# Kernel tuning notes

Measured on AMD Instinct MI355X. Metric: run time of the kernel, lower is better.

The kernel has to match this reference:

```python
import jax, jax.numpy as jnp
import numpy as np

TEMPERATURE = 0.5
EPS = 1e-8
NEG = -1e30  # effectively -inf for masked logits


def _l2norm(x):
    n = jnp.sqrt(jnp.sum(x * x, axis=1, keepdims=True))
    return x / jnp.maximum(n, EPS)


def setup_inputs() -> dict:
    key = jax.random.key(0)
    ks = jax.random.split(key, 4)
    N, D = 2048, 128
    return {f"projection_image_aug{i+1}": jax.random.normal(ks[i], (N, D), dtype=jnp.float32)
            for i in range(4)}


def reference(projection_image_aug1, projection_image_aug2,
              projection_image_aug3, projection_image_aug4):
    zs = [projection_image_aug1.astype(jnp.float32),
          projection_image_aug2.astype(jnp.float32),
          projection_image_aug3.astype(jnp.float32),
          projection_image_aug4.astype(jnp.float32)]
    N = zs[0].shape[0]
    k = len(zs)
    z = jnp.concatenate(zs[:2], axis=0)        # [2N, D]
    z_all = jnp.concatenate(zs, axis=0)        # [kN, D]
    # cosine sim via normalize + matmul (same math as broadcast CosineSimilarity)
    sim = _l2norm(z) @ _l2norm(z_all).T / TEMPERATURE   # [2N, kN]

    rows = jnp.arange(2 * N)
    half = rows // N                 # 0 for first N rows, 1 for second
    idx = rows % N
    cols = jnp.arange(k * N)
    block = cols // N
    # mask: diagonal entries of every N-block except the target block (1-half)
    diag = (cols[None, :] % N) == idx[:, None]
    mask = diag & (block[None, :] != (1 - half)[:, None])
    sim_m = jnp.where(mask, NEG, sim)
    # positive column: aug2 partner for rows<N, aug1 partner for rows>=N
    target_col = (1 - half) * N + idx
    pos = jnp.take_along_axis(sim_m, target_col[:, None], axis=1)[:, 0]
    # cross_entropy(reduction='sum') / (2N)
    loss = jnp.sum(jax.nn.logsumexp(sim_m, axis=1) - pos) / (2 * N)
    return loss
```

## Files before the change

### kernel.cpp

```cpp
#include <hip/hip_runtime.h>
#include <hip/hip_bf16.h>


#define NN      2048
#define DD      128
#define TWO_N   4096
#define FOUR_N  8192
#define BM      128
#define BN      128
#define CT      64

using frag_ab = __attribute__((ext_vector_type(8))) short;
using f32x4   = __attribute__((ext_vector_type(4))) float;

__device__ inline void gl_lds16(const short* g, short* l) {
  __builtin_amdgcn_global_load_lds(
      (const __attribute__((address_space(1))) void*)g,
      (__attribute__((address_space(3))) void*)l, 16, 0, 0);
}

__device__ inline int swz(int chunk) {
  return (chunk & ~15) | ((chunk & 15) ^ ((chunk >> 4) & 15));
}

__global__ __launch_bounds__(256) void knorm(const float* __restrict__ p0,
                                             const float* __restrict__ p1,
                                             const float* __restrict__ p2,
                                             const float* __restrict__ p3,
                                             short* __restrict__ Bn,
                                             float* __restrict__ out) {
  if (blockIdx.x == 0 && threadIdx.x == 0) out[0] = 0.0f;
  int wave = threadIdx.x >> 6, lane = threadIdx.x & 63;
  int row = blockIdx.x * 4 + wave;
  int q = row >> 11, idx = row & (NN - 1);
  const float* src = (q == 0) ? p0 : (q == 1) ? p1 : (q == 2) ? p2 : p3;
  const float2* s2 = (const float2*)(src + (size_t)idx * DD);
  float2 v = s2[lane];
  float ss = v.x * v.x + v.y * v.y;
  #pragma unroll
  for (int sh = 1; sh < 64; sh <<= 1) ss += __shfl_xor(ss, sh, 64);
  float inv = 1.0f / fmaxf(sqrtf(ss), 1e-8f);
  __hip_bfloat162 o;
  o.x = __float2bfloat16(v.x * inv);
  o.y = __float2bfloat16(v.y * inv);
  ((__hip_bfloat162*)(Bn + (size_t)row * DD))[lane] = o;
}

__global__ __launch_bounds__(256) void kgemm(const short* __restrict__ Bn,
                                             float* __restrict__ pS) {
  __shared__ short sA[BM * DD];
  __shared__ short sB[BN * DD];
  __shared__ float sS[BM][2];

  int t = threadIdx.x, wave = t >> 6, lane = t & 63;
  int quad = lane >> 4, l16 = lane & 15;

  const short* gA = Bn + (size_t)blockIdx.x * BM * DD;
  const short* gB = Bn + (size_t)blockIdx.y * BN * DD;
  #pragma unroll
  for (int i = 0; i < 8; ++i) {
    int c0 = i * 256 + wave * 64;
    gl_lds16(gA + (size_t)swz(c0 + lane) * 8, sA + (size_t)c0 * 8);
    gl_lds16(gB + (size_t)swz(c0 + lane) * 8, sB + (size_t)c0 * 8);
  }
  __syncthreads();

  int rowHalf = wave >> 1, colHalf = wave & 1;
  f32x4 acc[4][4];
  #pragma unroll
  for (int rf = 0; rf < 4; ++rf)
    #pragma unroll
    for (int cf = 0; cf < 4; ++cf) acc[rf][cf] = (f32x4){0.f, 0.f, 0.f, 0.f};

  #pragma unroll
  for (int k = 0; k < 4; ++k) {
    frag_ab a[4], b[4];
    #pragma unroll
    for (int rf = 0; rf < 4; ++rf) {
      int r_ = rowHalf * 64 + rf * 16 + l16;
      a[rf] = *(const frag_ab*)&sA[(size_t)((r_ << 4) | ((k * 4 + quad) ^ l16)) * 8];
    }
    #pragma unroll
    for (int cf = 0; cf < 4; ++cf) {
      int r_ = colHalf * 64 + cf * 16 + l16;
      b[cf] = *(const frag_ab*)&sB[(size_t)((r_ << 4) | ((k * 4 + quad) ^ l16)) * 8];
    }
    #pragma unroll
    for (int rf = 0; rf < 4; ++rf)
      #pragma unroll
      for (int cf = 0; cf < 4; ++cf)
        acc[rf][cf] = __builtin_amdgcn_mfma_f32_16x16x32_bf16(a[rf], b[cf], acc[rf][cf], 0, 0, 0);
  }

  int grBase = blockIdx.x * BM;
  #pragma unroll
  for (int rf = 0; rf < 4; ++rf) {
    #pragma unroll
    for (int r = 0; r < 4; ++r) {
      int rowLocal = rowHalf * 64 + rf * 16 + quad * 4 + r;
      float s = 0.f;
      #pragma unroll
      for (int cf = 0; cf < 4; ++cf)
        s += __expf(fmaf(acc[rf][cf][r], 2.0f, -2.0f));
      #pragma unroll
      for (int sh = 1; sh < 16; sh <<= 1) s += __shfl_xor(s, sh, 64);
      if (l16 == 0) sS[rowLocal][colHalf] = s;
    }
  }
  __syncthreads();
  if (t < BM)
    pS[(size_t)(grBase + t) * CT + blockIdx.y] = sS[t][0] + sS[t][1];
}

__global__ __launch_bounds__(256) void kfin(const short* __restrict__ Bn,
                                            const float* __restrict__ pS,
                                            float* __restrict__ out) {
  int t = threadIdx.x, wave = t >> 6, lane = t & 63;
  int grBase = blockIdx.x * BM;
  __shared__ float sRed[4];

  float wloss = 0.f;
  for (int rr = wave; rr < BM; rr += 4) {
    int gr = grBase + rr;
    int idx = gr & (NN - 1), half = gr >> 11;
    float S = pS[(size_t)gr * CT + lane];
    #pragma unroll
    for (int sh = 1; sh < 64; sh <<= 1) S += __shfl_xor(S, sh, 64);
    unsigned int ua = ((const unsigned int*)(Bn + (size_t)gr * DD))[lane];
    unsigned int ub = ((const unsigned int*)(Bn + (size_t)((1 - half) * NN + idx) * DD))[lane];
    unsigned int uc = ((const unsigned int*)(Bn + (size_t)(2 * NN + idx) * DD))[lane];
    unsigned int ud = ((const unsigned int*)(Bn + (size_t)(3 * NN + idx) * DD))[lane];
    float a0 = __uint_as_float((ua & 0xffffu) << 16), a1 = __uint_as_float(ua & 0xffff0000u);
    float b0 = __uint_as_float((ub & 0xffffu) << 16), b1 = __uint_as_float(ub & 0xffff0000u);
    float c0 = __uint_as_float((uc & 0xffffu) << 16), c1 = __uint_as_float(uc & 0xffff0000u);
    float d0 = __uint_as_float((ud & 0xffffu) << 16), d1 = __uint_as_float(ud & 0xffff0000u);
    float daa = a0 * a0 + a1 * a1;
    float dab = a0 * b0 + a1 * b1;
    float dac = a0 * c0 + a1 * c1;
    float dad = a0 * d0 + a1 * d1;
    #pragma unroll
    for (int sh = 1; sh < 64; sh <<= 1) {
      daa += __shfl_xor(daa, sh, 64);
      dab += __shfl_xor(dab, sh, 64);
      dac += __shfl_xor(dac, sh, 64);
      dad += __shfl_xor(dad, sh, 64);
    }
    float Sc = S - __expf(fmaf(daa, 2.0f, -2.0f))
                 - __expf(fmaf(dac, 2.0f, -2.0f))
                 - __expf(fmaf(dad, 2.0f, -2.0f));
    float loss = (2.0f + __logf(Sc)) - 2.0f * dab;
    if (lane == 0) wloss += loss;
  }
  if (lane == 0) sRed[wave] = wloss;
  __syncthreads();
  if (t == 0)
    atomicAdd(out, (sRed[0] + sRed[1] + sRed[2] + sRed[3]) * (1.0f / (float)TWO_N));
}

extern "C" void kernel_launch(void* const* d_in, const int* in_sizes, int n_in,
                              void* d_out, int out_size, void* d_ws, size_t ws_size,
                              hipStream_t stream) {
  (void)in_sizes; (void)n_in; (void)out_size; (void)ws_size;
  const float* p0 = (const float*)d_in[0];
  const float* p1 = (const float*)d_in[1];
  const float* p2 = (const float*)d_in[2];
  const float* p3 = (const float*)d_in[3];

  short* Bn = (short*)d_ws;
  float* pS = (float*)((char*)d_ws + (size_t)FOUR_N * DD * sizeof(short));
  float* out = (float*)d_out;

  knorm<<<FOUR_N / 4, 256, 0, stream>>>(p0, p1, p2, p3, Bn, out);
  kgemm<<<dim3(TWO_N / BM, FOUR_N / BN), 256, 0, stream>>>(Bn, pS);
  kfin<<<TWO_N / BM, 256, 0, stream>>>(Bn, pS, out);
}
```

Baseline: 110.4 us.

## Make GEMM blocks persistent over column tiles with double-buffered B loads

Each GEMM block now sweeps 8 consecutive 128-column tiles instead of one. The A fragments stay in registers across the sweep, and the next B tile is prefetched into a second LDS buffer while the current tile is multiplied. Per-row exp sums accumulate in registers, so the partial-sum buffer shrinks from 64 to 8 entries per row and the final kernel reduces fewer values. The aim is to cut block launch overhead, repeated A loads and the partial-sum traffic. The cost is a grid of only 256 blocks at one block per CU with 4 waves, which may leave MFMA and exp latency poorly hidden.

New measurement: 122.8 us. 11.2% more time.

```diff
diff --git a/kernel.cpp b/kernel.cpp
--- a/kernel.cpp
+++ b/kernel.cpp
@@ -8,7 +8,8 @@
 #define FOUR_N  8192
 #define BM      128
 #define BN      128
-#define CT      64
+#define GT      8
+#define CTG     8
 
 using frag_ab = __attribute__((ext_vector_type(8))) short;
 using f32x4   = __attribute__((ext_vector_type(4))) float;
@@ -46,70 +47,101 @@
   ((__hip_bfloat162*)(Bn + (size_t)row * DD))[lane] = o;
 }
 
-__global__ __launch_bounds__(256) void kgemm(const short* __restrict__ Bn,
-                                             float* __restrict__ pS) {
+__global__ __launch_bounds__(256, 1) void kgemm(const short* __restrict__ Bn,
+                                                float* __restrict__ pS) {
   __shared__ short sA[BM * DD];
-  __shared__ short sB[BN * DD];
+  __shared__ short sB[2][BN * DD];
   __shared__ float sS[BM][2];
 
   int t = threadIdx.x, wave = t >> 6, lane = t & 63;
   int quad = lane >> 4, l16 = lane & 15;
+  int rowHalf = wave >> 1, colHalf = wave & 1;
 
   const short* gA = Bn + (size_t)blockIdx.x * BM * DD;
-  const short* gB = Bn + (size_t)blockIdx.y * BN * DD;
+  const short* gB0 = Bn + (size_t)blockIdx.y * (GT * BN) * DD;
+
   #pragma unroll
   for (int i = 0; i < 8; ++i) {
     int c0 = i * 256 + wave * 64;
     gl_lds16(gA + (size_t)swz(c0 + lane) * 8, sA + (size_t)c0 * 8);
-    gl_lds16(gB + (size_t)swz(c0 + lane) * 8, sB + (size_t)c0 * 8);
+    gl_lds16(gB0 + (size_t)swz(c0 + lane) * 8, sB[0] + (size_t)c0 * 8);
   }
   __syncthreads();
 
-  int rowHalf = wave >> 1, colHalf = wave & 1;
-  f32x4 acc[4][4];
-  #pragma unroll
-  for (int rf = 0; rf < 4; ++rf)
-    #pragma unroll
-    for (int cf = 0; cf < 4; ++cf) acc[rf][cf] = (f32x4){0.f, 0.f, 0.f, 0.f};
-
-  #pragma unroll
-  for (int k = 0; k < 4; ++k) {
-    frag_ab a[4], b[4];
+  frag_ab a[4][4];
+  #pragma unroll
+  for (int k = 0; k < 4; ++k)
     #pragma unroll
     for (int rf = 0; rf < 4; ++rf) {
       int r_ = rowHalf * 64 + rf * 16 + l16;
-      a[rf] = *(const frag_ab*)&sA[(size_t)((r_ << 4) | ((k * 4 + quad) ^ l16)) * 8];
-    }
-    #pragma unroll
-    for (int cf = 0; cf < 4; ++cf) {
-      int r_ = colHalf * 64 + cf * 16 + l16;
-      b[cf] = *(const frag_ab*)&sB[(size_t)((r_ << 4) | ((k * 4 + quad) ^ l16)) * 8];
-    }
+      a[k][rf] = *(const frag_ab*)&sA[(size_t)((r_ << 4) | ((k * 4 + quad) ^ l16)) * 8];
+    }
+
+  float sAcc[4][4];
+  #pragma unroll
+  for (int rf = 0; rf < 4; ++rf)
+    #pragma unroll
+    for (int r = 0; r < 4; ++r) sAcc[rf][r] = 0.f;
+
+  #pragma unroll
+  for (int g = 0; g < GT; ++g) {
+    if (g < GT - 1) {
+      const short* gBn = gB0 + (size_t)(g + 1) * BN * DD;
+      short* dst = sB[(g + 1) & 1];
+      #pragma unroll
+      for (int i = 0; i < 8; ++i) {
+        int c0 = i * 256 + wave * 64;
+        gl_lds16(gBn + (size_t)swz(c0 + lane) * 8, dst + (size_t)c0 * 8);
+      }
+    }
+    const short* sBg = sB[g & 1];
+
+    f32x4 acc[4][4];
     #pragma unroll
     for (int rf = 0; rf < 4; ++rf)
       #pragma unroll
-      for (int cf = 0; cf < 4; ++cf)
-        acc[rf][cf] = __builtin_amdgcn_mfma_f32_16x16x32_bf16(a[rf], b[cf], acc[rf][cf], 0, 0, 0);
+      for (int cf = 0; cf < 4; ++cf) acc[rf][cf] = (f32x4){0.f, 0.f, 0.f, 0.f};
+
+    #pragma unroll
+    for (int k = 0; k < 4; ++k) {
+      frag_ab b[4];
+      #pragma unroll
+      for (int cf = 0; cf < 4; ++cf) {
+        int r_ = colHalf * 64 + cf * 16 + l16;
+        b[cf] = *(const frag_ab*)&sBg[(size_t)((r_ << 4) | ((k * 4 + quad) ^ l16)) * 8];
+      }
+      #pragma unroll
+      for (int rf = 0; rf < 4; ++rf)
+        #pragma unroll
+        for (int cf = 0; cf < 4; ++cf)
+          acc[rf][cf] = __builtin_amdgcn_mfma_f32_16x16x32_bf16(a[k][rf], b[cf], acc[rf][cf], 0, 0, 0);
+    }
+
+    #pragma unroll
+    for (int rf = 0; rf < 4; ++rf)
+      #pragma unroll
+      for (int r = 0; r < 4; ++r) {
+        float s = 0.f;
+        #pragma unroll
+        for (int cf = 0; cf < 4; ++cf)
+          s += __expf(fmaf(acc[rf][cf][r], 2.0f, -2.0f));
+        sAcc[rf][r] += s;
+      }
+    __syncthreads();
   }
 
-  int grBase = blockIdx.x * BM;
-  #pragma unroll
-  for (int rf = 0; rf < 4; ++rf) {
+  #pragma unroll
+  for (int rf = 0; rf < 4; ++rf)
     #pragma unroll
     for (int r = 0; r < 4; ++r) {
-      int rowLocal = rowHalf * 64 + rf * 16 + quad * 4 + r;
-      float s = 0.f;
-      #pragma unroll
-      for (int cf = 0; cf < 4; ++cf)
-        s += __expf(fmaf(acc[rf][cf][r], 2.0f, -2.0f));
+      float s = sAcc[rf][r];
       #pragma unroll
       for (int sh = 1; sh < 16; sh <<= 1) s += __shfl_xor(s, sh, 64);
-      if (l16 == 0) sS[rowLocal][colHalf] = s;
-    }
-  }
+      if (l16 == 0) sS[rowHalf * 64 + rf * 16 + quad * 4 + r][colHalf] = s;
+    }
   __syncthreads();
   if (t < BM)
-    pS[(size_t)(grBase + t) * CT + blockIdx.y] = sS[t][0] + sS[t][1];
+    pS[(size_t)(blockIdx.x * BM + t) * CTG + blockIdx.y] = sS[t][0] + sS[t][1];
 }
 
 __global__ __launch_bounds__(256) void kfin(const short* __restrict__ Bn,
@@ -123,9 +155,9 @@
   for (int rr = wave; rr < BM; rr += 4) {
     int gr = grBase + rr;
     int idx = gr & (NN - 1), half = gr >> 11;
-    float S = pS[(size_t)gr * CT + lane];
-    #pragma unroll
-    for (int sh = 1; sh < 64; sh <<= 1) S += __shfl_xor(S, sh, 64);
+    float S = (lane < CTG) ? pS[(size_t)gr * CTG + lane] : 0.f;
+    #pragma unroll
+    for (int sh = 1; sh < 8; sh <<= 1) S += __shfl_xor(S, sh, 64);
     unsigned int ua = ((const unsigned int*)(Bn + (size_t)gr * DD))[lane];
     unsigned int ub = ((const unsigned int*)(Bn + (size_t)((1 - half) * NN + idx) * DD))[lane];
     unsigned int uc = ((const unsigned int*)(Bn + (size_t)(2 * NN + idx) * DD))[lane];
@@ -171,6 +203,6 @@
   float* out = (float*)d_out;
 
   knorm<<<FOUR_N / 4, 256, 0, stream>>>(p0, p1, p2, p3, Bn, out);
-  kgemm<<<dim3(TWO_N / BM, FOUR_N / BN), 256, 0, stream>>>(Bn, pS);
+  kgemm<<<dim3(TWO_N / BM, CTG), 256, 0, stream>>>(Bn, pS);
   kfin<<<TWO_N / BM, 256, 0, stream>>>(Bn, pS, out);
 }
```
